# Optimization experiments

Hardware: AMD Instinct MI355X
Metric: run time of the kernel (lower is better)

The kernel has to match this reference:

```python
import jax, jax.numpy as jnp
import numpy as np
from jax import lax

NUM_CNNS = 300
INPUT_LEN = 608
NUM_CLASSES = 50
FILTER = 19
POOL = 7
HIDDEN = 100
BATCH = 256
L_CONV = INPUT_LEN - FILTER + 1          # 590
L_POOL = (L_CONV - POOL) // POOL + 1     # 84
EPS = 1e-5


def setup_inputs() -> dict:
    key = jax.random.key(0)
    ks = jax.random.split(key, 24)
    U, H = NUM_CNNS, HIDDEN
    d = {}
    d["x"] = jax.random.normal(ks[0], (BATCH, 4, INPUT_LEN), dtype=jnp.float32)
    # conv1: grouped Conv1d(4*U -> U, k=19, groups=U) on replicated input == dense Conv1d(4 -> U)
    d["w1"] = jax.random.normal(ks[1], (U, 4, FILTER), dtype=jnp.float32) * 0.1
    d["b1"] = jax.random.normal(ks[2], (U,), dtype=jnp.float32) * 0.05
    d["g1"] = jax.random.uniform(ks[3], (U,), dtype=jnp.float32, minval=0.5, maxval=1.5)
    d["be1"] = jax.random.normal(ks[4], (U,), dtype=jnp.float32) * 0.05
    d["m1"] = jax.random.normal(ks[5], (U,), dtype=jnp.float32) * 0.05
    d["v1"] = jax.random.uniform(ks[6], (U,), dtype=jnp.float32, minval=0.5, maxval=1.5)
    # grouped 1x1 conv: per-unit Linear 84 -> 100
    d["w2"] = jax.random.normal(ks[7], (U, H, L_POOL), dtype=jnp.float32) * (1.0 / np.sqrt(L_POOL))
    d["b2"] = jax.random.normal(ks[8], (U, H), dtype=jnp.float32) * 0.05
    d["g2"] = jax.random.uniform(ks[9], (U, H), dtype=jnp.float32, minval=0.5, maxval=1.5)
    d["be2"] = jax.random.normal(ks[10], (U, H), dtype=jnp.float32) * 0.05
    d["m2"] = jax.random.normal(ks[11], (U, H), dtype=jnp.float32) * 0.05
    d["v2"] = jax.random.uniform(ks[12], (U, H), dtype=jnp.float32, minval=0.5, maxval=1.5)
    # grouped 1x1 conv: per-unit Linear 100 -> 1
    d["w3"] = jax.random.normal(ks[13], (U, H), dtype=jnp.float32) * (1.0 / np.sqrt(H))
    d["b3"] = jax.random.normal(ks[14], (U,), dtype=jnp.float32) * 0.05
    d["g3"] = jax.random.uniform(ks[15], (U,), dtype=jnp.float32, minval=0.5, maxval=1.5)
    d["be3"] = jax.random.normal(ks[16], (U,), dtype=jnp.float32) * 0.05
    d["m3"] = jax.random.normal(ks[17], (U,), dtype=jnp.float32) * 0.05
    d["v3"] = jax.random.uniform(ks[18], (U,), dtype=jnp.float32, minval=0.5, maxval=1.5)
    # final Linear(U -> num_classes)
    d["wf"] = jax.random.normal(ks[19], (NUM_CLASSES, U), dtype=jnp.float32) * (1.0 / np.sqrt(U))
    d["bf"] = jax.random.normal(ks[20], (NUM_CLASSES,), dtype=jnp.float32) * 0.05
    return d


def _bn(y, g, be, m, v):
    return (y - m) * (g * lax.rsqrt(v + EPS)) + be


def reference(x, w1, b1, g1, be1, m1, v1, w2, b2, g2, be2, m2, v2,
              w3, b3, g3, be3, m3, v3, wf, bf):
    # conv1 (replicate + grouped conv == dense conv over 4 channels)
    y = lax.conv_general_dilated(x, w1, window_strides=(1,), padding='VALID',
                                 dimension_numbers=('NCH', 'OIH', 'NCH'))  # [B,U,590]
    y = y + b1[None, :, None]
    y = _bn(y, g1[None, :, None], be1[None, :, None], m1[None, :, None], v1[None, :, None])
    y = jnp.exp(y)  # ExpActivation
    # MaxPool1d(7,7): 590 -> 84 (uses first 588 positions)
    B = y.shape[0]
    y = y[:, :, :L_POOL * POOL].reshape(B, NUM_CNNS, L_POOL, POOL).max(axis=-1)  # [B,U,84]
    # per-unit MLP 84 -> 100 (grouped 1x1 conv) + BN + ReLU (dropout is eval-mode identity)
    h = jnp.einsum('buf,uof->buo', y, w2) + b2[None]  # [B,U,100]
    h = _bn(h, g2[None], be2[None], m2[None], v2[None])
    h = jax.nn.relu(h)
    # per-unit 100 -> 1 + BN + ReLU
    z = jnp.einsum('buo,uo->bu', h, w3) + b3[None]  # [B,U]
    z = _bn(z, g3[None], be3[None], m3[None], v3[None])
    z = jax.nn.relu(z)
    # final Linear
    return z @ wf.T + bf
```

## Files before the change

### kernel.cpp

```cpp
#include <hip/hip_runtime.h>
#include <hip/hip_bf16.h>

#define BATCH    256
#define NU       300
#define LIN      608
#define FILT     19
#define LPOOL    84
#define POOL     7
#define HID      100
#define NCLS     50
#define EPS      1e-5f
#define KP       96
#define NP       112
#define LDK      104
#define WROW     104
#define WBROWS   320
#define TCHUNK   112
#define CROW     116
#define MTN      19
#define BH       128

typedef __attribute__((ext_vector_type(8))) short short8;
typedef __attribute__((ext_vector_type(4))) float float4v;

__device__ __forceinline__ unsigned short f2bf(float f) {
    unsigned u = __float_as_uint(f);
    u += 0x7fffu + ((u >> 16) & 1u);
    return (unsigned short)(u >> 16);
}
__device__ __forceinline__ float bf2f(unsigned short h) {
    return __uint_as_float(((unsigned)h) << 16);
}

__global__ void k_prep(const float* __restrict__ w1, const float* __restrict__ x,
                       unsigned short* __restrict__ Wbh,
                       unsigned short* __restrict__ Wbl,
                       unsigned int* __restrict__ xc)
{
    const int idx = blockIdx.x * 256 + threadIdx.x;
    const int NW = WBROWS * WROW;
    if (idx < NW) {
        const int u = idx / WROW, kk = idx - u * WROW;
        float wv = 0.f;
        if (u < NU && kk < 96) {
            const int c = kk / 24, tap = kk - 24 * c;
            if (tap < FILT) wv = w1[(u * 4 + c) * FILT + tap];
        }
        const unsigned short hi = f2bf(wv);
        Wbh[idx] = hi;
        Wbl[idx] = f2bf(wv - bf2f(hi));
    }
    const int j = idx - NW;
    if (j >= 0 && j < BATCH * 4 * LIN) {
        const float xv = x[j];
        const unsigned short hi = f2bf(xv);
        const unsigned short lo = f2bf(xv - bf2f(hi));
        xc[j] = (unsigned)hi | ((unsigned)lo << 16);
    }
}

__global__ __launch_bounds__(256, 2)
void k_conv4(const unsigned short* __restrict__ Wbh,
             const unsigned short* __restrict__ Wbl,
             const unsigned int* __restrict__ xc,
             const float* __restrict__ b1, const float* __restrict__ g1,
             const float* __restrict__ be1, const float* __restrict__ m1,
             const float* __restrict__ v1,
             unsigned short* __restrict__ ypool)
{
    __shared__ __align__(16) unsigned short Bh[TCHUNK * LDK];
    __shared__ __align__(16) unsigned short Bl[TCHUNK * LDK];
    __shared__ float Cs[2][16 * CROW];
    __shared__ float s1s[MTN * 16], c1s[MTN * 16];

    const int tid = threadIdx.x;
    const int b   = blockIdx.x;
    const int tc  = blockIdx.y;
    const int t0  = TCHUNK * tc;
    const int NT  = (tc == 5) ? 2 : 7;

    for (int i = tid; i < TCHUNK * 12; i += 256) {
        const int trow = i / 12;
        if (trow >= 16 * NT) continue;
        const int rem   = i - 12 * trow;
        const int c     = rem / 3;
        const int third = rem - 3 * c;
        const int kkb   = 24 * c + 8 * third;
        const int tt0   = t0 + trow + 8 * third;
        const unsigned int* src = xc + ((b * 4 + c) * LIN + tt0);

        unsigned int w[8];
        if (third < 2 && tt0 + 8 <= LIN) {
            const uint4 v0 = *(const uint4*)(src);
            const uint4 v1 = *(const uint4*)(src + 4);
            w[0] = v0.x; w[1] = v0.y; w[2] = v0.z; w[3] = v0.w;
            w[4] = v1.x; w[5] = v1.y; w[6] = v1.z; w[7] = v1.w;
        } else {
#pragma unroll
            for (int j = 0; j < 8; ++j) {
                const int tap = 8 * third + j;
                const int tt  = tt0 + j;
                unsigned int v = 0;
                if (tap < FILT && tt < LIN) v = src[j];
                w[j] = v;
            }
        }
        short8 hv, lv;
#pragma unroll
        for (int j = 0; j < 8; ++j) {
            hv[j] = (short)(w[j] & 0xffffu);
            lv[j] = (short)(w[j] >> 16);
        }
        *(short8*)(&Bh[trow * LDK + kkb]) = hv;
        *(short8*)(&Bl[trow * LDK + kkb]) = lv;
    }
    for (int i = tid; i < MTN * 16; i += 256) {
        if (i < NU) {
            const float s = g1[i] * rsqrtf(v1[i] + EPS);
            s1s[i] = s;
            c1s[i] = (b1[i] - m1[i]) * s + be1[i];
        } else { s1s[i] = 0.f; c1s[i] = 0.f; }
    }
    __syncthreads();

    const int lane = tid & 63;
    const int n    = lane & 15;
    const int quad = lane >> 4;
    const int wave = tid >> 6;

    short8 bh[2][3], bl[2][3];
#pragma unroll
    for (int kk2 = 0; kk2 < 2; ++kk2) {
        const int nt = wave + 4 * kk2;
        if (nt < NT) {
#pragma unroll
            for (int s = 0; s < 3; ++s) {
                bh[kk2][s] = *(const short8*)(&Bh[(16 * nt + n) * LDK + 32 * s + 8 * quad]);
                bl[kk2][s] = *(const short8*)(&Bl[(16 * nt + n) * LDK + 32 * s + 8 * quad]);
            }
        }
    }

    const int ep_p = tid & 15;
    const int ep_u = tid >> 4;

    short8 afh[3], afl[3], nfh[3], nfl[3];
    {
        const unsigned short* wrh = Wbh + (size_t)n * WROW;
        const unsigned short* wrl = Wbl + (size_t)n * WROW;
#pragma unroll
        for (int s = 0; s < 3; ++s) {
            afh[s] = *(const short8*)(wrh + 32 * s + 8 * quad);
            afl[s] = *(const short8*)(wrl + 32 * s + 8 * quad);
        }
    }

    for (int mt = 0; mt < MTN; ++mt) {
        const int mtn = (mt + 1 < MTN) ? mt + 1 : mt;
        const unsigned short* wrh = Wbh + (size_t)(mtn * 16 + n) * WROW;
        const unsigned short* wrl = Wbl + (size_t)(mtn * 16 + n) * WROW;
#pragma unroll
        for (int s = 0; s < 3; ++s) {
            nfh[s] = *(const short8*)(wrh + 32 * s + 8 * quad);
            nfl[s] = *(const short8*)(wrl + 32 * s + 8 * quad);
        }

        float4v acc[2];
#pragma unroll
        for (int kk2 = 0; kk2 < 2; ++kk2) {
            acc[kk2] = (float4v){0.f, 0.f, 0.f, 0.f};
            if (wave + 4 * kk2 < NT) {
#pragma unroll
                for (int s = 0; s < 3; ++s)
                    acc[kk2] = __builtin_amdgcn_mfma_f32_16x16x32_bf16(
                        afh[s], bh[kk2][s], acc[kk2], 0, 0, 0);
#pragma unroll
                for (int s = 0; s < 3; ++s)
                    acc[kk2] = __builtin_amdgcn_mfma_f32_16x16x32_bf16(
                        afh[s], bl[kk2][s], acc[kk2], 0, 0, 0);
#pragma unroll
                for (int s = 0; s < 3; ++s)
                    acc[kk2] = __builtin_amdgcn_mfma_f32_16x16x32_bf16(
                        afl[s], bh[kk2][s], acc[kk2], 0, 0, 0);
            }
        }

        float* cbuf = Cs[mt & 1];
#pragma unroll
        for (int kk2 = 0; kk2 < 2; ++kk2) {
            const int nt = wave + 4 * kk2;
            if (nt < NT) {
#pragma unroll
                for (int r = 0; r < 4; ++r)
                    cbuf[(4 * quad + r) * CROW + 16 * nt + n] = acc[kk2][r];
            }
        }
        __syncthreads();

        const int uglob = mt * 16 + ep_u;
        if (uglob < NU) {
            const int p = 16 * tc + ep_p;
            unsigned short outv = 0;
            if (p < LPOOL) {
                const float* row = &cbuf[ep_u * CROW + 7 * ep_p];
                float mx = row[0];
#pragma unroll
                for (int j = 1; j < 7; ++j) mx = fmaxf(mx, row[j]);
                outv = f2bf(__expf(fmaf(mx, s1s[uglob], c1s[uglob])));
            }
            if (p < KP)
                ypool[((size_t)uglob * BATCH + b) * KP + p] = outv;
        }

#pragma unroll
        for (int s = 0; s < 3; ++s) { afh[s] = nfh[s]; afl[s] = nfl[s]; }
    }
}

__global__ __launch_bounds__(256, 3)
void k_mlp(const unsigned short* __restrict__ ypool,
           const float* __restrict__ w2, const float* __restrict__ b2,
           const float* __restrict__ g2, const float* __restrict__ be2,
           const float* __restrict__ m2, const float* __restrict__ v2,
           const float* __restrict__ w3, const float* __restrict__ b3,
           const float* __restrict__ g3, const float* __restrict__ be3,
           const float* __restrict__ m3, const float* __restrict__ v3,
           float* __restrict__ zbuf)
{
    __shared__ __align__(16) unsigned short As[NP * LDK];
    __shared__ __align__(16) unsigned short Bs[BH * LDK];
    __shared__ __align__(16) float4 cs4[NP];

    const int tid = threadIdx.x;
    const int u   = blockIdx.x;
    const int b0  = blockIdx.y * BH;

    {
        const float* src = w2 + (size_t)u * HID * LPOOL;
        for (int c = tid; c < HID * (LPOOL / 4); c += 256) {
            const int o  = c / (LPOOL / 4);
            const int kc = (c % (LPOOL / 4)) * 4;
            const float4 v = *(const float4*)(src + o * LPOOL + kc);
            unsigned short* d = &As[o * LDK + kc];
            d[0] = f2bf(v.x); d[1] = f2bf(v.y); d[2] = f2bf(v.z); d[3] = f2bf(v.w);
        }
        for (int c = tid; c < HID * 6; c += 256) {
            const int o = c / 6, kc = LPOOL + (c % 6) * 2;
            *(unsigned*)(&As[o * LDK + kc]) = 0;
        }
        for (int c = tid; c < (NP - HID) * (KP / 2); c += 256) {
            const int o = HID + c / (KP / 2), kc = (c % (KP / 2)) * 2;
            *(unsigned*)(&As[o * LDK + kc]) = 0;
        }
    }
    {
        const unsigned short* ys = ypool + ((size_t)u * BATCH + b0) * KP;
        for (int c = tid; c < BH * (KP / 8); c += 256) {
            const int n  = c / (KP / 8);
            const int kc = (c % (KP / 8)) * 8;
            *(short8*)(&Bs[n * LDK + kc]) = *(const short8*)(ys + n * KP + kc);
        }
    }
    if (tid < NP) {
        float4 cv = {0.f, 0.f, 0.f, 0.f};
        if (tid < HID) {
            const int uo = u * HID + tid;
            const float s = g2[uo] * rsqrtf(v2[uo] + EPS);
            cv.x = s;
            cv.y = (b2[uo] - m2[uo]) * s + be2[uo];
            cv.z = w3[uo];
        }
        cs4[tid] = cv;
    }
    __syncthreads();

    const int lane = tid & 63;
    const int wave = tid >> 6;
    const int col  = lane & 15;
    const int quad = lane >> 4;

    short8 bf_[2][3];
#pragma unroll
    for (int j = 0; j < 2; ++j) {
        const int brow = 16 * (2 * wave + j) + col;
#pragma unroll
        for (int s = 0; s < 3; ++s)
            bf_[j][s] = *(const short8*)(&Bs[brow * LDK + 32 * s + 8 * quad]);
    }

    float zp0 = 0.f, zp1 = 0.f;
#pragma unroll
    for (int mt = 0; mt < 7; ++mt) {
        short8 af[3];
#pragma unroll
        for (int s = 0; s < 3; ++s)
            af[s] = *(const short8*)(&As[(16 * mt + col) * LDK + 32 * s + 8 * quad]);

        float4v a0 = {0.f, 0.f, 0.f, 0.f}, a1 = {0.f, 0.f, 0.f, 0.f};
#pragma unroll
        for (int s = 0; s < 3; ++s) {
            a0 = __builtin_amdgcn_mfma_f32_16x16x32_bf16(af[s], bf_[0][s], a0, 0, 0, 0);
            a1 = __builtin_amdgcn_mfma_f32_16x16x32_bf16(af[s], bf_[1][s], a1, 0, 0, 0);
        }
#pragma unroll
        for (int r = 0; r < 4; ++r) {
            const float4 cv = cs4[16 * mt + 4 * quad + r];
            zp0 = fmaf(fmaxf(fmaf(a0[r], cv.x, cv.y), 0.f), cv.z, zp0);
            zp1 = fmaf(fmaxf(fmaf(a1[r], cv.x, cv.y), 0.f), cv.z, zp1);
        }
    }

    zp0 += __shfl_xor(zp0, 16); zp0 += __shfl_xor(zp0, 32);
    zp1 += __shfl_xor(zp1, 16); zp1 += __shfl_xor(zp1, 32);

    if (quad == 0) {
        const float s3 = g3[u] * rsqrtf(v3[u] + EPS);
        const float c3 = (b3[u] - m3[u]) * s3 + be3[u];
        const int bA = b0 + 16 * (2 * wave + 0) + col;
        const int bB = b0 + 16 * (2 * wave + 1) + col;
        zbuf[(size_t)u * BATCH + bA] = fmaxf(fmaf(zp0, s3, c3), 0.f);
        zbuf[(size_t)u * BATCH + bB] = fmaxf(fmaf(zp1, s3, c3), 0.f);
    }
}

__global__ __launch_bounds__(256, 4)
void k_final(const float* __restrict__ zbuf, const float* __restrict__ wf,
             const float* __restrict__ bf, float* __restrict__ out)
{
    __shared__ float red[4][64];
    const int nc   = blockIdx.x;
    const int bq   = blockIdx.y;
    const int lane = threadIdx.x & 63;
    const int wave = threadIdx.x >> 6;
    const int b    = bq * 64 + lane;

    float a0 = 0.f, a1 = 0.f, a2 = 0.f;
    const int u0 = wave * 75;
#pragma unroll 5
    for (int i = 0; i < 75; i += 3) {
        a0 = fmaf(zbuf[(size_t)(u0 + i + 0) * BATCH + b], wf[nc * NU + u0 + i + 0], a0);
        a1 = fmaf(zbuf[(size_t)(u0 + i + 1) * BATCH + b], wf[nc * NU + u0 + i + 1], a1);
        a2 = fmaf(zbuf[(size_t)(u0 + i + 2) * BATCH + b], wf[nc * NU + u0 + i + 2], a2);
    }
    red[wave][lane] = (a0 + a1) + a2;
    __syncthreads();
    if (threadIdx.x < 64) {
        const float s = (red[0][lane] + red[1][lane]) + (red[2][lane] + red[3][lane]);
        out[(size_t)b * NCLS + nc] = s + bf[nc];
    }
}

extern "C" void kernel_launch(void* const* d_in, const int* in_sizes, int n_in,
                              void* d_out, int out_size, void* d_ws, size_t ws_size,
                              hipStream_t stream)
{
    const float* x   = (const float*)d_in[0];
    const float* w1  = (const float*)d_in[1];
    const float* b1  = (const float*)d_in[2];
    const float* g1  = (const float*)d_in[3];
    const float* be1 = (const float*)d_in[4];
    const float* m1  = (const float*)d_in[5];
    const float* v1  = (const float*)d_in[6];
    const float* w2  = (const float*)d_in[7];
    const float* b2  = (const float*)d_in[8];
    const float* g2  = (const float*)d_in[9];
    const float* be2 = (const float*)d_in[10];
    const float* m2  = (const float*)d_in[11];
    const float* v2  = (const float*)d_in[12];
    const float* w3  = (const float*)d_in[13];
    const float* b3  = (const float*)d_in[14];
    const float* g3  = (const float*)d_in[15];
    const float* be3 = (const float*)d_in[16];
    const float* m3  = (const float*)d_in[17];
    const float* v3  = (const float*)d_in[18];
    const float* wf  = (const float*)d_in[19];
    const float* bf  = (const float*)d_in[20];

    unsigned short* ypool = (unsigned short*)d_ws;
    float* zbuf = (float*)((char*)d_ws + 14745600);
    unsigned short* Wbh = (unsigned short*)((char*)d_ws + 15052800);
    unsigned short* Wbl = (unsigned short*)((char*)d_ws + 15119360);
    unsigned int*   xc  = (unsigned int*)((char*)d_ws + 15185920);

    const int prep_elems = WBROWS * WROW + BATCH * 4 * LIN;
    k_prep<<<(prep_elems + 255) / 256, 256, 0, stream>>>(w1, x, Wbh, Wbl, xc);

    dim3 gc(BATCH, 6);
    k_conv4<<<gc, 256, 0, stream>>>(Wbh, Wbl, xc, b1, g1, be1, m1, v1, ypool);

    dim3 gm(NU, BATCH / BH);
    k_mlp<<<gm, 256, 0, stream>>>(ypool, w2, b2, g2, be2, m2, v2,
                                  w3, b3, g3, be3, m3, v3, zbuf);

    dim3 gf(NCLS, 4);
    k_final<<<gf, 256, 0, stream>>>(zbuf, wf, bf, (float*)d_out);
}
```

Measured before the change: 181.2 us.

## Split conv work by unit tile per wave to remove block-wide barriers

Each wave now owns whole unit tiles (mt strided by 4) and computes all seven time tiles itself, so the pooling epilogue needs only wave-local LDS staging fenced by workgroup fences instead of a __syncthreads per unit tile. B fragments are re-read from LDS per tile rather than held in registers, and weight prefetching is dropped. This removes the 19 block barriers per block and the load imbalance across waves on the tail time chunk. In exchange it adds LDS read traffic, loses the weight prefetch, and the 19 tiles split unevenly across 4 waves (5,5,5,4).

```diff
diff --git a/kernel.cpp b/kernel.cpp
--- a/kernel.cpp
+++ b/kernel.cpp
@@ -60,7 +60,7 @@
 }
 
 __global__ __launch_bounds__(256, 2)
-void k_conv4(const unsigned short* __restrict__ Wbh,
+void k_conv5(const unsigned short* __restrict__ Wbh,
              const unsigned short* __restrict__ Wbl,
              const unsigned int* __restrict__ xc,
              const float* __restrict__ b1, const float* __restrict__ g1,
@@ -70,7 +70,7 @@
 {
     __shared__ __align__(16) unsigned short Bh[TCHUNK * LDK];
     __shared__ __align__(16) unsigned short Bl[TCHUNK * LDK];
-    __shared__ float Cs[2][16 * CROW];
+    __shared__ float Cs[4][8 * CROW];
     __shared__ float s1s[MTN * 16], c1s[MTN * 16];
 
     const int tid = threadIdx.x;
@@ -127,93 +127,80 @@
     const int n    = lane & 15;
     const int quad = lane >> 4;
     const int wave = tid >> 6;
-
-    short8 bh[2][3], bl[2][3];
-#pragma unroll
-    for (int kk2 = 0; kk2 < 2; ++kk2) {
-        const int nt = wave + 4 * kk2;
-        if (nt < NT) {
-#pragma unroll
-            for (int s = 0; s < 3; ++s) {
-                bh[kk2][s] = *(const short8*)(&Bh[(16 * nt + n) * LDK + 32 * s + 8 * quad]);
-                bl[kk2][s] = *(const short8*)(&Bl[(16 * nt + n) * LDK + 32 * s + 8 * quad]);
-            }
-        }
-    }
-
-    const int ep_p = tid & 15;
-    const int ep_u = tid >> 4;
-
-    short8 afh[3], afl[3], nfh[3], nfl[3];
-    {
-        const unsigned short* wrh = Wbh + (size_t)n * WROW;
-        const unsigned short* wrl = Wbl + (size_t)n * WROW;
+    float* Csw = Cs[wave];
+
+    for (int mt = wave; mt < MTN; mt += 4) {
+        const unsigned short* wrh = Wbh + (size_t)(mt * 16 + n) * WROW;
+        const unsigned short* wrl = Wbl + (size_t)(mt * 16 + n) * WROW;
+        short8 afh[3], afl[3];
 #pragma unroll
         for (int s = 0; s < 3; ++s) {
             afh[s] = *(const short8*)(wrh + 32 * s + 8 * quad);
             afl[s] = *(const short8*)(wrl + 32 * s + 8 * quad);
         }
-    }
-
-    for (int mt = 0; mt < MTN; ++mt) {
-        const int mtn = (mt + 1 < MTN) ? mt + 1 : mt;
-        const unsigned short* wrh = Wbh + (size_t)(mtn * 16 + n) * WROW;
-        const unsigned short* wrl = Wbl + (size_t)(mtn * 16 + n) * WROW;
-#pragma unroll
-        for (int s = 0; s < 3; ++s) {
-            nfh[s] = *(const short8*)(wrh + 32 * s + 8 * quad);
-            nfl[s] = *(const short8*)(wrl + 32 * s + 8 * quad);
-        }
-
-        float4v acc[2];
-#pragma unroll
-        for (int kk2 = 0; kk2 < 2; ++kk2) {
-            acc[kk2] = (float4v){0.f, 0.f, 0.f, 0.f};
-            if (wave + 4 * kk2 < NT) {
+
+        float4v acc[7];
+#pragma unroll
+        for (int nt = 0; nt < 7; ++nt) {
+            acc[nt] = (float4v){0.f, 0.f, 0.f, 0.f};
+            if (nt < NT) {
+                short8 bhf[3], blf[3];
+#pragma unroll
+                for (int s = 0; s < 3; ++s) {
+                    bhf[s] = *(const short8*)(&Bh[(16 * nt + n) * LDK + 32 * s + 8 * quad]);
+                    blf[s] = *(const short8*)(&Bl[(16 * nt + n) * LDK + 32 * s + 8 * quad]);
+                }
 #pragma unroll
                 for (int s = 0; s < 3; ++s)
-                    acc[kk2] = __builtin_amdgcn_mfma_f32_16x16x32_bf16(
-                        afh[s], bh[kk2][s], acc[kk2], 0, 0, 0);
+                    acc[nt] = __builtin_amdgcn_mfma_f32_16x16x32_bf16(
+                        afh[s], bhf[s], acc[nt], 0, 0, 0);
 #pragma unroll
                 for (int s = 0; s < 3; ++s)
-                    acc[kk2] = __builtin_amdgcn_mfma_f32_16x16x32_bf16(
-                        afh[s], bl[kk2][s], acc[kk2], 0, 0, 0);
+                    acc[nt] = __builtin_amdgcn_mfma_f32_16x16x32_bf16(
+                        afh[s], blf[s], acc[nt], 0, 0, 0);
 #pragma unroll
                 for (int s = 0; s < 3; ++s)
-                    acc[kk2] = __builtin_amdgcn_mfma_f32_16x16x32_bf16(
-                        afl[s], bh[kk2][s], acc[kk2], 0, 0, 0);
+                    acc[nt] = __builtin_amdgcn_mfma_f32_16x16x32_bf16(
+                        afl[s], bhf[s], acc[nt], 0, 0, 0);
             }
         }
 
-        float* cbuf = Cs[mt & 1];
-#pragma unroll
-        for (int kk2 = 0; kk2 < 2; ++kk2) {
-            const int nt = wave + 4 * kk2;
-            if (nt < NT) {
-#pragma unroll
-                for (int r = 0; r < 4; ++r)
-                    cbuf[(4 * quad + r) * CROW + 16 * nt + n] = acc[kk2][r];
+#pragma unroll
+        for (int half = 0; half < 2; ++half) {
+            __builtin_amdgcn_fence(__ATOMIC_ACQ_REL, "workgroup");
+            if ((quad >> 1) == half) {
+                const int lrow = (quad & 1) * 4;
+#pragma unroll
+                for (int nt = 0; nt < 7; ++nt) {
+                    if (nt < NT) {
+#pragma unroll
+                        for (int r = 0; r < 4; ++r)
+                            Csw[(lrow + r) * CROW + 16 * nt + n] = acc[nt][r];
+                    }
+                }
             }
-        }
-        __syncthreads();
-
-        const int uglob = mt * 16 + ep_u;
-        if (uglob < NU) {
-            const int p = 16 * tc + ep_p;
-            unsigned short outv = 0;
-            if (p < LPOOL) {
-                const float* row = &cbuf[ep_u * CROW + 7 * ep_p];
-                float mx = row[0];
-#pragma unroll
-                for (int j = 1; j < 7; ++j) mx = fmaxf(mx, row[j]);
-                outv = f2bf(__expf(fmaf(mx, s1s[uglob], c1s[uglob])));
+            __builtin_amdgcn_fence(__ATOMIC_ACQ_REL, "workgroup");
+#pragma unroll
+            for (int rep = 0; rep < 2; ++rep) {
+                const int id = rep * 64 + lane;
+                const int ul = id & 7;
+                const int p  = id >> 3;
+                const int uglob = mt * 16 + half * 8 + ul;
+                if (uglob < NU) {
+                    const int pg = 16 * tc + p;
+                    unsigned short outv = 0;
+                    if (pg < LPOOL) {
+                        const float* row = &Csw[ul * CROW + 7 * p];
+                        float mx = row[0];
+#pragma unroll
+                        for (int j = 1; j < 7; ++j) mx = fmaxf(mx, row[j]);
+                        outv = f2bf(__expf(fmaf(mx, s1s[uglob], c1s[uglob])));
+                    }
+                    if (pg < KP)
+                        ypool[((size_t)uglob * BATCH + b) * KP + pg] = outv;
+                }
             }
-            if (p < KP)
-                ypool[((size_t)uglob * BATCH + b) * KP + p] = outv;
-        }
-
-#pragma unroll
-        for (int s = 0; s < 3; ++s) { afh[s] = nfh[s]; afl[s] = nfl[s]; }
+        }
     }
 }
 
@@ -386,7 +373,7 @@
     k_prep<<<(prep_elems + 255) / 256, 256, 0, stream>>>(w1, x, Wbh, Wbl, xc);
 
     dim3 gc(BATCH, 6);
-    k_conv4<<<gc, 256, 0, stream>>>(Wbh, Wbl, xc, b1, g1, be1, m1, v1, ypool);
+    k_conv5<<<gc, 256, 0, stream>>>(Wbh, Wbl, xc, b1, g1, be1, m1, v1, ypool);
 
     dim3 gm(NU, BATCH / BH);
     k_mlp<<<gm, 256, 0, stream>>>(ypool, w2, b2, g2, be2, m2, v2,
```

After: 166.3 us. 1.09x faster.
